# Performance work log

Measured on AMD Instinct MI355X. Metric: run time of the kernel, lower is better.

## Reference

```python
import jax, jax.numpy as jnp
import numpy as np

# fixed-point config (matches init_kwargs)
DIM, H = 768, 12
DHEAD = DIM // H
DATA_W, DATA_F = 32, 16        # input activation quantizer
WQ = WK = WV = WP = (16, 8)    # weight quantizers (width, frac)
BQ = BK = BV = BP = (16, 8)    # bias quantizers
DQ = DK = DV = DS = DZ = (16, 8)  # activation quantizers after each stage
OUT_W, OUT_F = 32, 8


def qfix(x, width, frac):
    """Fixed-point integer quantizer: round to 2^-frac grid, clamp to signed width."""
    scale = jnp.float32(2.0 ** frac)
    lo = -(2.0 ** (width - 1))
    hi = 2.0 ** (width - 1) - 1
    return jnp.clip(jnp.round(x * scale), lo, hi) / scale


def setup_inputs() -> dict:
    key = jax.random.key(0)
    ks = jax.random.split(key, 5)
    return {
        "q_in": jax.random.normal(ks[0], (2, 2048, DIM), dtype=jnp.float32),
        "wqkv": jax.random.normal(ks[1], (3 * DIM, DIM), dtype=jnp.float32) * 0.05,
        "bqkv": jax.random.normal(ks[2], (3 * DIM,), dtype=jnp.float32) * 0.05,
        "wp": jax.random.normal(ks[3], (DIM, DIM), dtype=jnp.float32) * 0.05,
        "bp": jax.random.normal(ks[4], (DIM,), dtype=jnp.float32) * 0.05,
    }


def reference(q_in, wqkv, bqkv, wp, bp):
    B, N, _ = q_in.shape
    # per-head weight split: wqkv -> (H, 3*DHEAD, DIM), rows [0:d]=q, [d:2d]=k, [2d:3d]=v
    w = wqkv.reshape(H, 3 * DHEAD, DIM)
    b = bqkv.reshape(H, 3 * DHEAD)
    wq_, wk_, wv_ = w[:, :DHEAD], w[:, DHEAD:2 * DHEAD], w[:, 2 * DHEAD:]
    bq_, bk_, bv_ = b[:, :DHEAD], b[:, DHEAD:2 * DHEAD], b[:, 2 * DHEAD:]

    x = qfix(q_in, DATA_W, DATA_F)  # QuantizedLinear input quantization

    def qlin(wt, bt, wcfg, bcfg, ocfg):
        # y[b,h,n,e] = x[b,n,d] @ qw[h,e,d]^T + qb[h,e], then output quantize
        y = jnp.einsum('bnd,hed->bhne', x, qfix(wt, *wcfg)) + qfix(bt, *bcfg)[None, :, None, :]
        return qfix(y, *ocfg)

    q = qlin(wq_, bq_, WQ, BQ, DQ)  # (B,H,N,DHEAD)
    k = qlin(wk_, bk_, WK, BK, DK)
    v = qlin(wv_, bv_, WV, BV, DV)

    s = qfix(jnp.einsum('bhne,bhme->bhnm', q, k), *DS)   # (B,H,N,N) quantized scores
    z = qfix(jnp.einsum('bhnm,bhme->bhne', s, v), *DZ)   # (B,H,N,DHEAD)

    # concat heads along feature dim (torch.cat dim=2)
    zc = z.transpose(0, 2, 1, 3).reshape(B, N, DIM)

    # quantized projection: input quantized with data_z cfg (idempotent here)
    out = jnp.einsum('bnd,ed->bne', qfix(zc, *DZ), qfix(wp, *WP)) + qfix(bp, *BP)
    return qfix(out, OUT_W, OUT_F)
```

## Files before the change

### kernel.cpp

```cpp
#include <hip/hip_runtime.h>


#define NTOK 4096
#define DIM  768
#define NH   12
#define DH   64
#define SEQ  2048
#define QKVD 2304
#define NBH  24
#define LSTR 72

typedef _Float16 half8 __attribute__((ext_vector_type(8)));
typedef _Float16 half4 __attribute__((ext_vector_type(4)));
typedef __fp16   fp16x2 __attribute__((ext_vector_type(2)));
typedef float floatx4 __attribute__((ext_vector_type(4)));
typedef float floatx16 __attribute__((ext_vector_type(16)));

__global__ __launch_bounds__(256) void prep(
    const float* __restrict__ X,
    const float* __restrict__ wqkv, const float* __restrict__ bqkv,
    const float* __restrict__ wp,   const float* __restrict__ bp,
    _Float16* __restrict__ Xh, _Float16* __restrict__ Xl,
    _Float16* __restrict__ W16, _Float16* __restrict__ Wp16,
    float* __restrict__ bq24, float* __restrict__ bp16)
{
    int i = blockIdx.x * 256 + threadIdx.x;
    int i4 = i * 4;
    if (i4 < NTOK * DIM) {
        float4 x = *(const float4*)(X + i4);
        float xi[4] = {x.x, x.y, x.z, x.w};
        half4 oh, ol;
#pragma unroll
        for (int j = 0; j < 4; ++j) {
            float v = rintf(xi[j] * 65536.0f);
            float h = rintf(v * (1.0f / 2048.0f));
            ((_Float16*)&oh)[j] = (_Float16)h;
            ((_Float16*)&ol)[j] = (_Float16)(v - 2048.0f * h);
        }
        *(half4*)(Xh + i4) = oh;
        *(half4*)(Xl + i4) = ol;
    }
    if (i4 < QKVD * DIM) {
        float4 w = *(const float4*)(wqkv + i4);
        half4 o = {(_Float16)rintf(w.x * 256.0f), (_Float16)rintf(w.y * 256.0f),
                   (_Float16)rintf(w.z * 256.0f), (_Float16)rintf(w.w * 256.0f)};
        *(half4*)(W16 + i4) = o;
    }
    if (i4 < DIM * DIM) {
        float4 w = *(const float4*)(wp + i4);
        half4 o = {(_Float16)rintf(w.x * 256.0f), (_Float16)rintf(w.y * 256.0f),
                   (_Float16)rintf(w.z * 256.0f), (_Float16)rintf(w.w * 256.0f)};
        *(half4*)(Wp16 + i4) = o;
    }
    if (i < QKVD) bq24[i] = rintf(bqkv[i] * 256.0f) * 65536.0f;
    if (i < DIM)  bp16[i] = rintf(bp[i] * 256.0f) * 256.0f;
}

__global__ __launch_bounds__(256, 4) void qkv_mfma(
    const _Float16* __restrict__ Xh, const _Float16* __restrict__ Xl,
    const _Float16* __restrict__ W16, const float* __restrict__ bq24,
    _Float16* __restrict__ Q16, _Float16* __restrict__ K16,
    _Float16* __restrict__ Vt16)
{
    __shared__ __align__(16) _Float16 Ah[64 * LSTR];
    __shared__ __align__(16) _Float16 Al[64 * LSTR];
    __shared__ __align__(16) _Float16 Bs[128 * LSTR];
    const int t = threadIdx.x;
    const int w = t >> 6, lane = t & 63;
    const int l31 = lane & 31, hi = lane >> 5;
    const int wr = w >> 1;
    const int wc = w & 1;
    const int m0 = blockIdx.x * 64;
    const int col0 = blockIdx.y * 128;

    floatx16 acch[2], accl[2];
#pragma unroll
    for (int ct = 0; ct < 2; ++ct)
#pragma unroll
        for (int r = 0; r < 16; ++r) { acch[ct][r] = 0.f; accl[ct][r] = 0.f; }

    for (int k0 = 0; k0 < DIM; k0 += 64) {
        __syncthreads();
#pragma unroll
        for (int i = 0; i < 2; ++i) {
            int id = t + 256 * i;
            int r = id >> 3, c8 = id & 7;
            *(half8*)(&Ah[r * LSTR + c8 * 8]) =
                *(const half8*)(Xh + (size_t)(m0 + r) * DIM + k0 + c8 * 8);
            *(half8*)(&Al[r * LSTR + c8 * 8]) =
                *(const half8*)(Xl + (size_t)(m0 + r) * DIM + k0 + c8 * 8);
        }
#pragma unroll
        for (int i = 0; i < 4; ++i) {
            int id = t + 256 * i;
            int r = id >> 3, c8 = id & 7;
            *(half8*)(&Bs[r * LSTR + c8 * 8]) =
                *(const half8*)(W16 + (size_t)(col0 + r) * DIM + k0 + c8 * 8);
        }
        __syncthreads();
#pragma unroll
        for (int i = 0; i < 4; ++i) {
            half8 ah = *(const half8*)(&Ah[(32 * wr + l31) * LSTR + 16 * i + 8 * hi]);
            half8 al = *(const half8*)(&Al[(32 * wr + l31) * LSTR + 16 * i + 8 * hi]);
#pragma unroll
            for (int ct = 0; ct < 2; ++ct) {
                half8 bf = *(const half8*)(&Bs[(64 * wc + 32 * ct + l31) * LSTR + 16 * i + 8 * hi]);
                acch[ct] = __builtin_amdgcn_mfma_f32_32x32x16_f16(ah, bf, acch[ct], 0, 0, 0);
                accl[ct] = __builtin_amdgcn_mfma_f32_32x32x16_f16(al, bf, accl[ct], 0, 0, 0);
            }
        }
    }

    const int b_ = m0 >> 11;
    const int nbase = (m0 & 2047) + 32 * wr;
#pragma unroll
    for (int ct = 0; ct < 2; ++ct) {
        const int c = col0 + 64 * wc + 32 * ct + l31;
        const int h = c / 192;
        const int jj = c % 192;
        const int kind = jj >> 6;
        const int e = jj & 63;
        const int bh = b_ * NH + h;
        const float bb = bq24[c];
        float qv[16];
#pragma unroll
        for (int r = 0; r < 16; ++r) {
            float y = fmaf(2048.0f, acch[ct][r], accl[ct][r]) + bb;
            float q = rintf(y * (1.0f / 65536.0f));
            qv[r] = fminf(fmaxf(q, -32768.0f), 32767.0f);
        }
        if (kind == 2) {
#pragma unroll
            for (int g = 0; g < 4; ++g) {
                int nv = nbase + 16 * (g >> 1) + 8 * hi + 4 * (g & 1);
                half4 o = {(_Float16)qv[4 * g + 0], (_Float16)qv[4 * g + 1],
                           (_Float16)qv[4 * g + 2], (_Float16)qv[4 * g + 3]};
                *(half4*)(Vt16 + ((size_t)bh * DH + e) * SEQ + nv) = o;
            }
        } else {
            _Float16* dst = (kind == 0) ? Q16 : K16;
#pragma unroll
            for (int r = 0; r < 16; ++r) {
                int er = (r & 3) + 8 * (r >> 2) + 4 * hi;
                dst[((size_t)bh * SEQ + nbase + er) * DH + e] = (_Float16)qv[r];
            }
        }
    }
}

__global__ __launch_bounds__(256, 3) void attention_mfma(
    const _Float16* __restrict__ Q16, const _Float16* __restrict__ K16,
    const _Float16* __restrict__ Vt16,
    _Float16* __restrict__ Zh16, _Float16* __restrict__ Zl16)
{
    __shared__ __align__(16) char smem[64 * LSTR * 2 * 2];
    _Float16* Ks = (_Float16*)smem;
    _Float16* Vs = Ks + 64 * LSTR;
    float* scr = (float*)smem;

    const int t = threadIdx.x;
    const int bh = blockIdx.x;
    const int qt = blockIdx.y;
    const int w = t >> 6, lane = t & 63;
    const int l31 = lane & 31, hi = lane >> 5;
    const int wj = w & 1;
    const int wi = w >> 1;
    const _Float16* Qg = Q16 + ((size_t)bh * SEQ + qt * 64) * DH;
    const _Float16* Kg = K16 + (size_t)bh * SEQ * DH;
    const _Float16* Vg = Vt16 + (size_t)bh * DH * SEQ;

    half8 qf[4];
#pragma unroll
    for (int i = 0; i < 4; ++i)
        qf[i] = *(const half8*)(Qg + (32 * wj + l31) * DH + 16 * i + 8 * hi);

    floatx16 acc0h, acc0l, acc1h, acc1l;
#pragma unroll
    for (int r = 0; r < 16; ++r) { acc0h[r] = 0.f; acc0l[r] = 0.f; acc1h[r] = 0.f; acc1l[r] = 0.f; }

    for (int m0 = 0; m0 < SEQ; m0 += 64) {
        __syncthreads();
        {
            int r = t >> 3, k8 = t & 7;
            *(half8*)(&Ks[r * LSTR + k8 * 8]) =
                *(const half8*)(Kg + (size_t)(m0 + r) * DH + k8 * 8);
            *(half8*)(&Vs[r * LSTR + k8 * 8]) =
                *(const half8*)(Vg + (size_t)r * SEQ + m0 + k8 * 8);
            int t2 = t + 256; int r2 = t2 >> 3, k82 = t2 & 7;
            *(half8*)(&Ks[r2 * LSTR + k82 * 8]) =
                *(const half8*)(Kg + (size_t)(m0 + r2) * DH + k82 * 8);
            *(half8*)(&Vs[r2 * LSTR + k82 * 8]) =
                *(const half8*)(Vg + (size_t)r2 * SEQ + m0 + k82 * 8);
        }
        __syncthreads();

        floatx16 sc;
#pragma unroll
        for (int r = 0; r < 16; ++r) sc[r] = 0.f;
#pragma unroll
        for (int i = 0; i < 4; ++i) {
            half8 kf = *(const half8*)(&Ks[(32 * wi + l31) * LSTR + 16 * i + 8 * hi]);
            sc = __builtin_amdgcn_mfma_f32_32x32x16_f16(kf, qf[i], sc, 0, 0, 0);
        }

        float hh[16], ll[16];
#pragma unroll
        for (int r = 0; r < 16; ++r) {
            float v = rintf(sc[r] * 0.00390625f);
            v = fminf(fmaxf(v, -32768.0f), 32767.0f);
            float h = rintf(v * (1.0f / 2048.0f));
            hh[r] = h;
            ll[r] = fmaf(-2048.0f, h, v);
        }
        int dwh[4][2], dwl[4][2];
        union { fp16x2 h; int i; } cv;
#pragma unroll
        for (int g = 0; g < 4; ++g) {
            cv.h = __builtin_amdgcn_cvt_pkrtz(hh[4 * g + 0], hh[4 * g + 1]); dwh[g][0] = cv.i;
            cv.h = __builtin_amdgcn_cvt_pkrtz(hh[4 * g + 2], hh[4 * g + 3]); dwh[g][1] = cv.i;
            cv.h = __builtin_amdgcn_cvt_pkrtz(ll[4 * g + 0], ll[4 * g + 1]); dwl[g][0] = cv.i;
            cv.h = __builtin_amdgcn_cvt_pkrtz(ll[4 * g + 2], ll[4 * g + 3]); dwl[g][1] = cv.i;
        }

        half8 vf[2][2];
#pragma unroll
        for (int et = 0; et < 2; ++et)
#pragma unroll
            for (int c = 0; c < 2; ++c)
                vf[et][c] = *(const half8*)(&Vs[(32 * et + l31) * LSTR + 32 * wi + 16 * c + 8 * hi]);
#pragma unroll
        for (int c = 0; c < 2; ++c) {
            union { int b[4]; half8 v; } ubh, ubl;
            ubh.b[0] = dwh[2 * c][0];     ubh.b[1] = dwh[2 * c][1];
            ubh.b[2] = dwh[2 * c + 1][0]; ubh.b[3] = dwh[2 * c + 1][1];
            ubl.b[0] = dwl[2 * c][0];     ubl.b[1] = dwl[2 * c][1];
            ubl.b[2] = dwl[2 * c + 1][0]; ubl.b[3] = dwl[2 * c + 1][1];
            acc0h = __builtin_amdgcn_mfma_f32_32x32x16_f16(vf[0][c], ubh.v, acc0h, 0, 0, 0);
            acc0l = __builtin_amdgcn_mfma_f32_32x32x16_f16(vf[0][c], ubl.v, acc0l, 0, 0, 0);
            acc1h = __builtin_amdgcn_mfma_f32_32x32x16_f16(vf[1][c], ubh.v, acc1h, 0, 0, 0);
            acc1l = __builtin_amdgcn_mfma_f32_32x32x16_f16(vf[1][c], ubl.v, acc1l, 0, 0, 0);
        }
    }

    float zfh[16], zfl[16];
    {
        __syncthreads();
#pragma unroll
        for (int r = 0; r < 16; ++r) {
            int er = (r & 3) + 8 * (r >> 2) + 4 * hi;
            float sendh = wi ? acc0h[r] : acc1h[r];
            scr[((wj * 2 + (1 - wi)) * 32 + er) * 33 + l31] = sendh;
        }
        __syncthreads();
#pragma unroll
        for (int r = 0; r < 16; ++r) {
            int er = (r & 3) + 8 * (r >> 2) + 4 * hi;
            float keeph = wi ? acc1h[r] : acc0h[r];
            zfh[r] = keeph + scr[((wj * 2 + wi) * 32 + er) * 33 + l31];
        }
        __syncthreads();
#pragma unroll
        for (int r = 0; r < 16; ++r) {
            int er = (r & 3) + 8 * (r >> 2) + 4 * hi;
            float sendl = wi ? acc0l[r] : acc1l[r];
            scr[((wj * 2 + (1 - wi)) * 32 + er) * 33 + l31] = sendl;
        }
        __syncthreads();
#pragma unroll
        for (int r = 0; r < 16; ++r) {
            int er = (r & 3) + 8 * (r >> 2) + 4 * hi;
            float keepl = wi ? acc1l[r] : acc0l[r];
            zfl[r] = keepl + scr[((wj * 2 + wi) * 32 + er) * 33 + l31];
        }
    }

    const int b_ = bh / NH, h = bh % NH;
    const int n = qt * 64 + 32 * wj + l31;
    const size_t rowoff = ((size_t)b_ * SEQ + n) * DIM + h * DH;
#pragma unroll
    for (int g = 0; g < 4; ++g) {
        int e0 = 32 * wi + 8 * g + 4 * hi;
        half4 ph, pl;
#pragma unroll
        for (int j = 0; j < 4; ++j) {
            int r = 4 * g + j;
            float zint = fmaf(2048.0f, zfh[r], zfl[r]);
            float zq = rintf(zint * 0.00390625f);
            zq = fminf(fmaxf(zq, -32768.0f), 32767.0f);
            float zdh = rintf(zq * (1.0f / 2048.0f));
            ((_Float16*)&ph)[j] = (_Float16)zdh;
            ((_Float16*)&pl)[j] = (_Float16)(zq - 2048.0f * zdh);
        }
        *(half4*)(Zh16 + rowoff + e0) = ph;
        *(half4*)(Zl16 + rowoff + e0) = pl;
    }
}

__global__ __launch_bounds__(256) void out_mfma(
    const _Float16* __restrict__ Zh, const _Float16* __restrict__ Zl,
    const _Float16* __restrict__ Wp16, const float* __restrict__ bp16,
    float* __restrict__ O)
{
    __shared__ __align__(16) _Float16 Ah[64 * LSTR];
    __shared__ __align__(16) _Float16 Al[64 * LSTR];
    __shared__ __align__(16) _Float16 Bs[128 * LSTR];
    const int t = threadIdx.x;
    const int wave = t >> 6, lane = t & 63;
    const int lrow = lane & 15, quad = lane >> 4;
    const int m0 = blockIdx.y * 64;
    const int col0 = blockIdx.x * 128;

    floatx4 acch[4][2], accl[4][2];
#pragma unroll
    for (int fm = 0; fm < 4; ++fm)
#pragma unroll
        for (int fn = 0; fn < 2; ++fn) {
            acch[fm][fn] = (floatx4){0.f, 0.f, 0.f, 0.f};
            accl[fm][fn] = (floatx4){0.f, 0.f, 0.f, 0.f};
        }

    for (int k0 = 0; k0 < DIM; k0 += 64) {
        __syncthreads();
#pragma unroll
        for (int i = 0; i < 2; ++i) {
            int id = t + 256 * i;
            int r = id >> 3, c8 = id & 7;
            *(half8*)(&Ah[r * LSTR + c8 * 8]) =
                *(const half8*)(Zh + (size_t)(m0 + r) * DIM + k0 + c8 * 8);
            *(half8*)(&Al[r * LSTR + c8 * 8]) =
                *(const half8*)(Zl + (size_t)(m0 + r) * DIM + k0 + c8 * 8);
        }
#pragma unroll
        for (int i = 0; i < 4; ++i) {
            int id = t + 256 * i;
            int r = id >> 3, c8 = id & 7;
            *(half8*)(&Bs[r * LSTR + c8 * 8]) =
                *(const half8*)(Wp16 + (size_t)(col0 + r) * DIM + k0 + c8 * 8);
        }
        __syncthreads();
#pragma unroll
        for (int kk = 0; kk < 64; kk += 32) {
            half8 bf[2];
#pragma unroll
            for (int fn = 0; fn < 2; ++fn)
                bf[fn] = *(const half8*)(&Bs[(wave * 32 + fn * 16 + lrow) * LSTR + kk + quad * 8]);
#pragma unroll
            for (int fm = 0; fm < 4; ++fm) {
                half8 ah = *(const half8*)(&Ah[(fm * 16 + lrow) * LSTR + kk + quad * 8]);
                half8 al = *(const half8*)(&Al[(fm * 16 + lrow) * LSTR + kk + quad * 8]);
#pragma unroll
                for (int fn = 0; fn < 2; ++fn) {
                    acch[fm][fn] = __builtin_amdgcn_mfma_f32_16x16x32_f16(ah, bf[fn], acch[fm][fn], 0, 0, 0);
                    accl[fm][fn] = __builtin_amdgcn_mfma_f32_16x16x32_f16(al, bf[fn], accl[fm][fn], 0, 0, 0);
                }
            }
        }
    }

#pragma unroll
    for (int fn = 0; fn < 2; ++fn) {
        const int c = col0 + wave * 32 + fn * 16 + lrow;
        const float bb = bp16[c];
#pragma unroll
        for (int fm = 0; fm < 4; ++fm)
#pragma unroll
            for (int rg = 0; rg < 4; ++rg) {
                float y = fmaf(2048.0f, acch[fm][fn][rg], accl[fm][fn][rg]) + bb;
                float o = rintf(y * 0.00390625f) * 0.00390625f;
                int r = m0 + fm * 16 + quad * 4 + rg;
                O[(size_t)r * DIM + c] = o;
            }
    }
}

extern "C" void kernel_launch(void* const* d_in, const int* in_sizes, int n_in,
                              void* d_out, int out_size, void* d_ws, size_t ws_size,
                              hipStream_t stream) {
    const float* q_in = (const float*)d_in[0];
    const float* wqkv = (const float*)d_in[1];
    const float* bqkv = (const float*)d_in[2];
    const float* wp   = (const float*)d_in[3];
    const float* bp   = (const float*)d_in[4];

    char* w = (char*)d_ws;
    _Float16* W16  = (_Float16*)w;  w += (size_t)QKVD * DIM * 2;
    _Float16* Wp16 = (_Float16*)w;  w += (size_t)DIM * DIM * 2;
    float* bq24    = (float*)w;     w += QKVD * 4;
    float* bp16    = (float*)w;     w += DIM * 4;
    _Float16* Xh   = (_Float16*)w;  w += (size_t)NTOK * DIM * 2;
    _Float16* Xl   = (_Float16*)w;  w += (size_t)NTOK * DIM * 2;
    _Float16* Q16  = (_Float16*)w;  w += (size_t)NBH * SEQ * DH * 2;
    _Float16* K16  = (_Float16*)w;  w += (size_t)NBH * SEQ * DH * 2;
    _Float16* Vt16 = (_Float16*)w;  w += (size_t)NBH * SEQ * DH * 2;
    _Float16* Zh16 = (_Float16*)w;  w += (size_t)NTOK * DIM * 2;
    _Float16* Zl16 = (_Float16*)w;  w += (size_t)NTOK * DIM * 2;
    (void)ws_size; (void)in_sizes; (void)n_in; (void)out_size;

    prep<<<dim3(NTOK * DIM / 4 / 256), 256, 0, stream>>>(
        q_in, wqkv, bqkv, wp, bp, Xh, Xl, W16, Wp16, bq24, bp16);
    qkv_mfma<<<dim3(NTOK / 64, QKVD / 128), 256, 0, stream>>>(
        Xh, Xl, W16, bq24, Q16, K16, Vt16);
    attention_mfma<<<dim3(NBH, SEQ / 64), 256, 0, stream>>>(Q16, K16, Vt16, Zh16, Zl16);
    out_mfma<<<dim3(DIM / 128, NTOK / 64), 256, 0, stream>>>(
        Zh16, Zl16, Wp16, bp16, (float*)d_out);
}
```

Baseline: 183.5 us.

## Double-buffer K/V tiles in attention with register prefetch and MFMA priority

The attention kernel now keeps two K/V shared-memory buffers and loads the next tile's K and V from global memory into registers before computing the current tile. The prefetched data is written to the alternate buffer after the MFMAs, which removes one of the two barriers per iteration and hides global load latency behind compute. It also raises wave priority around the MFMA blocks with s_setprio. The cost is double the LDS footprint (about 36 KB) and more registers, which may hurt the 3-blocks-per-CU occupancy target.

```diff
diff --git a/kernel.cpp b/kernel.cpp
--- a/kernel.cpp
+++ b/kernel.cpp
@@ -9,6 +9,7 @@
 #define QKVD 2304
 #define NBH  24
 #define LSTR 72
+#define KVBUF (64 * LSTR * 2 * 2)
 
 typedef _Float16 half8 __attribute__((ext_vector_type(8)));
 typedef _Float16 half4 __attribute__((ext_vector_type(4)));
@@ -153,9 +154,7 @@
     const _Float16* __restrict__ Vt16,
     _Float16* __restrict__ Zh16, _Float16* __restrict__ Zl16)
 {
-    __shared__ __align__(16) char smem[64 * LSTR * 2 * 2];
-    _Float16* Ks = (_Float16*)smem;
-    _Float16* Vs = Ks + 64 * LSTR;
+    __shared__ __align__(16) char smem[2 * KVBUF];
     float* scr = (float*)smem;
 
     const int t = threadIdx.x;
@@ -165,6 +164,7 @@
     const int l31 = lane & 31, hi = lane >> 5;
     const int wj = w & 1;
     const int wi = w >> 1;
+    const int sr = t >> 3, sk8 = t & 7;
     const _Float16* Qg = Q16 + ((size_t)bh * SEQ + qt * 64) * DH;
     const _Float16* Kg = K16 + (size_t)bh * SEQ * DH;
     const _Float16* Vg = Vt16 + (size_t)bh * DH * SEQ;
@@ -174,34 +174,47 @@
     for (int i = 0; i < 4; ++i)
         qf[i] = *(const half8*)(Qg + (32 * wj + l31) * DH + 16 * i + 8 * hi);
 
+    half8 pk0, pk1, pv0, pv1;
+    pk0 = *(const half8*)(Kg + (size_t)sr * DH + sk8 * 8);
+    pk1 = *(const half8*)(Kg + (size_t)(sr + 32) * DH + sk8 * 8);
+    pv0 = *(const half8*)(Vg + (size_t)sr * SEQ + sk8 * 8);
+    pv1 = *(const half8*)(Vg + (size_t)(sr + 32) * SEQ + sk8 * 8);
+    {
+        _Float16* Ks = (_Float16*)smem;
+        _Float16* Vs = Ks + 64 * LSTR;
+        *(half8*)(&Ks[sr * LSTR + sk8 * 8]) = pk0;
+        *(half8*)(&Ks[(sr + 32) * LSTR + sk8 * 8]) = pk1;
+        *(half8*)(&Vs[sr * LSTR + sk8 * 8]) = pv0;
+        *(half8*)(&Vs[(sr + 32) * LSTR + sk8 * 8]) = pv1;
+    }
+
     floatx16 acc0h, acc0l, acc1h, acc1l;
 #pragma unroll
     for (int r = 0; r < 16; ++r) { acc0h[r] = 0.f; acc0l[r] = 0.f; acc1h[r] = 0.f; acc1l[r] = 0.f; }
 
-    for (int m0 = 0; m0 < SEQ; m0 += 64) {
-        __syncthreads();
-        {
-            int r = t >> 3, k8 = t & 7;
-            *(half8*)(&Ks[r * LSTR + k8 * 8]) =
-                *(const half8*)(Kg + (size_t)(m0 + r) * DH + k8 * 8);
-            *(half8*)(&Vs[r * LSTR + k8 * 8]) =
-                *(const half8*)(Vg + (size_t)r * SEQ + m0 + k8 * 8);
-            int t2 = t + 256; int r2 = t2 >> 3, k82 = t2 & 7;
-            *(half8*)(&Ks[r2 * LSTR + k82 * 8]) =
-                *(const half8*)(Kg + (size_t)(m0 + r2) * DH + k82 * 8);
-            *(half8*)(&Vs[r2 * LSTR + k82 * 8]) =
-                *(const half8*)(Vg + (size_t)r2 * SEQ + m0 + k82 * 8);
-        }
-        __syncthreads();
+    for (int it = 0; it < 32; ++it) {
+        _Float16* Ks = (_Float16*)(smem + (it & 1) * KVBUF);
+        _Float16* Vs = Ks + 64 * LSTR;
+        __syncthreads();
+
+        if (it < 31) {
+            const int mn = (it + 1) * 64;
+            pk0 = *(const half8*)(Kg + (size_t)(mn + sr) * DH + sk8 * 8);
+            pk1 = *(const half8*)(Kg + (size_t)(mn + sr + 32) * DH + sk8 * 8);
+            pv0 = *(const half8*)(Vg + (size_t)sr * SEQ + mn + sk8 * 8);
+            pv1 = *(const half8*)(Vg + (size_t)(sr + 32) * SEQ + mn + sk8 * 8);
+        }
 
         floatx16 sc;
 #pragma unroll
         for (int r = 0; r < 16; ++r) sc[r] = 0.f;
+        __builtin_amdgcn_s_setprio(1);
 #pragma unroll
         for (int i = 0; i < 4; ++i) {
             half8 kf = *(const half8*)(&Ks[(32 * wi + l31) * LSTR + 16 * i + 8 * hi]);
             sc = __builtin_amdgcn_mfma_f32_32x32x16_f16(kf, qf[i], sc, 0, 0, 0);
         }
+        __builtin_amdgcn_s_setprio(0);
 
         float hh[16], ll[16];
 #pragma unroll
@@ -228,6 +241,7 @@
 #pragma unroll
             for (int c = 0; c < 2; ++c)
                 vf[et][c] = *(const half8*)(&Vs[(32 * et + l31) * LSTR + 32 * wi + 16 * c + 8 * hi]);
+        __builtin_amdgcn_s_setprio(1);
 #pragma unroll
         for (int c = 0; c < 2; ++c) {
             union { int b[4]; half8 v; } ubh, ubl;
@@ -239,6 +253,16 @@
             acc0l = __builtin_amdgcn_mfma_f32_32x32x16_f16(vf[0][c], ubl.v, acc0l, 0, 0, 0);
             acc1h = __builtin_amdgcn_mfma_f32_32x32x16_f16(vf[1][c], ubh.v, acc1h, 0, 0, 0);
             acc1l = __builtin_amdgcn_mfma_f32_32x32x16_f16(vf[1][c], ubl.v, acc1l, 0, 0, 0);
+        }
+        __builtin_amdgcn_s_setprio(0);
+
+        if (it < 31) {
+            _Float16* Kn = (_Float16*)(smem + ((it + 1) & 1) * KVBUF);
+            _Float16* Vn = Kn + 64 * LSTR;
+            *(half8*)(&Kn[sr * LSTR + sk8 * 8]) = pk0;
+            *(half8*)(&Kn[(sr + 32) * LSTR + sk8 * 8]) = pk1;
+            *(half8*)(&Vn[sr * LSTR + sk8 * 8]) = pv0;
+            *(half8*)(&Vn[(sr + 32) * LSTR + sk8 * 8]) = pv1;
         }
     }
 
```

After: 186.4 us. No clear change (+1.6%).
